# Kernel optimization log

Hardware: AMD Instinct MI355X
Metric: run time of the kernel (lower is better)

Reference implementation:

```python
import jax, jax.numpy as jnp
import numpy as np

N, D = 8192, 128
KERNEL_SCALE = 1.0     # constant baseline for kernel_scale
INV_TEMP = 1.0         # constant baseline: 1 / temperature
EMBED_DECAY = 0.0


def cauchy_kernel(x, y, scale):
    """Pairwise log-Cauchy kernel: -log(1 + ||x_i - y_j||^2 / scale). Shape [N, N]."""
    sq = (jnp.sum(x * x, axis=-1, keepdims=True)
          + jnp.sum(y * y, axis=-1)[None, :]
          - 2.0 * (x @ y.T))
    sq = jnp.maximum(sq, 0.0)  # guard tiny negatives from cancellation
    return -jnp.log1p(sq / scale)


def remove_diagonal(m):
    """[N, N] -> [N, N-1] dropping the diagonal (strided-view trick)."""
    n = m.shape[0]
    return m.reshape(-1)[1:].reshape(n - 1, n + 1)[:, :-1].reshape(n, n - 1)


def setup_inputs() -> dict:
    key = jax.random.key(0)
    k1, k2 = jax.random.split(key)
    z_x = jax.random.normal(k1, (N, D), dtype=jnp.float32)
    z_y = jax.random.normal(k2, (N, D), dtype=jnp.float32)
    return {"z_x": z_x, "z_y": z_y}


def reference(z_x, z_y):
    # pairwise log-likelihood-ratio logits
    logits = cauchy_kernel(z_x, z_y, KERNEL_SCALE) * INV_TEMP  # [N, N]
    pos_logits = jnp.diagonal(logits)[:, None]                 # [N, 1]
    neg_logits = remove_diagonal(logits)                       # [N, N-1]

    # "batch" baseline: log-mean-exp over all negative logits (scalar)
    log_baseline = jax.nn.logsumexp(neg_logits) - jnp.log(jnp.float32(neg_logits.size))

    pos_c = pos_logits - log_baseline
    neg_c = neg_logits - log_baseline

    # "kld" divergence (NCE/NWJ form): attraction on positives, exp-repulsion on negatives
    attraction = -jnp.mean(pos_c)
    repulsion = jnp.mean(jnp.exp(neg_c))

    # embedding prior = diagonal of kernel(z_y, zeros_like(z_y)) -> per-row log-density at origin
    embedding_prior = -jnp.log1p(jnp.sum(z_y * z_y, axis=-1) / KERNEL_SCALE)  # [N]
    embedding_decay = -EMBED_DECAY * jnp.mean(embedding_prior)

    loss = attraction + repulsion + embedding_decay
    return (jnp.mean(pos_logits), jnp.mean(neg_logits), log_baseline, loss)
```

## Files before the change

### kernel.cpp

```cpp
#include <hip/hip_runtime.h>
#include <hip/hip_bf16.h>

#define NN 8192
#define DD 128
#define NTB 64
#define STRIP 8

using floatx4 = __attribute__((ext_vector_type(4))) float;
using shortx8 = __attribute__((ext_vector_type(8))) short;
typedef unsigned short ushort_t;

typedef __attribute__((address_space(1))) const unsigned GlbU32;
typedef __attribute__((address_space(3))) unsigned LdsU32;

__device__ __forceinline__ unsigned bf16pair(float lo, float hi) {
    unsigned ulo = __float_as_uint(lo);
    ulo = (ulo + 0x7FFFu + ((ulo >> 16) & 1u)) >> 16;
    unsigned uhi = __float_as_uint(hi);
    uhi = (uhi + 0x7FFFu + ((uhi >> 16) & 1u)) & 0xFFFF0000u;
    return uhi | ulo;
}

__global__ void prep_kernel(const float* __restrict__ x, const float* __restrict__ y,
                            ushort_t* __restrict__ xb, ushort_t* __restrict__ yb,
                            float* __restrict__ xx, float* __restrict__ yy) {
    const int tid = threadIdx.x;
    const int r = blockIdx.x * 16 + (tid >> 4);
    const int c = tid & 15;
    const int sc = c ^ (r & 7);

    {
        const float4* xv = reinterpret_cast<const float4*>(x) + r * 32 + c * 2;
        const float4 a = xv[0], b = xv[1];
        uint4 u;
        u.x = bf16pair(a.x, a.y); u.y = bf16pair(a.z, a.w);
        u.z = bf16pair(b.x, b.y); u.w = bf16pair(b.z, b.w);
        reinterpret_cast<uint4*>(xb)[r * 16 + sc] = u;
        float s = a.x*a.x + a.y*a.y + a.z*a.z + a.w*a.w
                + b.x*b.x + b.y*b.y + b.z*b.z + b.w*b.w;
        #pragma unroll
        for (int off = 8; off; off >>= 1) s += __shfl_xor(s, off);
        if (c == 0) xx[r] = s;
    }
    {
        const float4* yv = reinterpret_cast<const float4*>(y) + r * 32 + c * 2;
        const float4 a = yv[0], b = yv[1];
        uint4 u;
        u.x = bf16pair(a.x, a.y); u.y = bf16pair(a.z, a.w);
        u.z = bf16pair(b.x, b.y); u.w = bf16pair(b.z, b.w);
        reinterpret_cast<uint4*>(yb)[r * 16 + sc] = u;
        float s = a.x*a.x + a.y*a.y + a.z*a.z + a.w*a.w
                + b.x*b.x + b.y*b.y + b.z*b.z + b.w*b.w;
        #pragma unroll
        for (int off = 8; off; off >>= 1) s += __shfl_xor(s, off);
        if (c == 0) yy[r] = s;
    }
}

__global__ __launch_bounds__(512, 4) void
tile_kernel(const ushort_t* __restrict__ xb, const ushort_t* __restrict__ yb,
            const float* __restrict__ xx, const float* __restrict__ yy,
            float* __restrict__ partials) {
    __shared__ __align__(16) ushort_t Bs[2][128 * DD];
    __shared__ float red[8][4];

    const int strip = blockIdx.x >> 6;
    const int by    = blockIdx.x & 63;
    const int bx0   = strip * STRIP;
    const int tid = threadIdx.x;
    const int wv = tid >> 6, lane = tid & 63;
    const int l15 = lane & 15, kq = lane >> 4;
    const int wr = (wv >> 1) * 32;
    const int wc = (wv & 1) * 64;
    const int lr = lane >> 4, lc = (lane & 15) * 8;

    #pragma unroll
    for (int it = 0; it < 4; ++it) {
        const int rbase = wv * 16 + it * 4;
        const ushort_t* gb = yb + ((size_t)(bx0 * 128 + rbase) + lr) * DD + lc;
        __builtin_amdgcn_global_load_lds((GlbU32*)gb, (LdsU32*)(&Bs[0][rbase * DD]), 16, 0, 0);
    }

    shortx8 a_reg[4][2];
    {
        const shortx8* xv = reinterpret_cast<const shortx8*>(xb);
        #pragma unroll
        for (int m = 0; m < 2; ++m) {
            const int ra = by * 128 + wr + m * 16 + l15;
            #pragma unroll
            for (int kk = 0; kk < 4; ++kk)
                a_reg[kk][m] = xv[ra * 16 + ((kk * 4 + kq) ^ (ra & 7))];
        }
    }
    float xv1[2][4];
    const int r0 = wr + kq * 4;
    #pragma unroll
    for (int m = 0; m < 2; ++m)
        #pragma unroll
        for (int j = 0; j < 4; ++j)
            xv1[m][j] = xx[by * 128 + r0 + m * 16 + j] + 1.0f;

    float s_l2 = 0.f, s_e = 0.f, p_l2 = 0.f, p_e = 0.f;

    __syncthreads();

    for (int t = 0; t < STRIP; ++t) {
        const int bx = bx0 + t;
        const int cur = t & 1;

        if (t + 1 < STRIP) {
            #pragma unroll
            for (int it = 0; it < 4; ++it) {
                const int rbase = wv * 16 + it * 4;
                const ushort_t* gb = yb + ((size_t)((bx + 1) * 128 + rbase) + lr) * DD + lc;
                __builtin_amdgcn_global_load_lds((GlbU32*)gb, (LdsU32*)(&Bs[cur ^ 1][rbase * DD]), 16, 0, 0);
            }
        }

        floatx4 acc[2][4];
        #pragma unroll
        for (int m = 0; m < 2; ++m)
            #pragma unroll
            for (int n = 0; n < 4; ++n)
                acc[m][n] = (floatx4){0.f, 0.f, 0.f, 0.f};

        const char* Bb = reinterpret_cast<const char*>(&Bs[cur][0]);
        #pragma unroll
        for (int kk = 0; kk < 4; ++kk) {
            shortx8 b[4];
            #pragma unroll
            for (int n = 0; n < 4; ++n) {
                const int rb = wc + n * 16 + l15;
                b[n] = *reinterpret_cast<const shortx8*>(Bb + ((rb * 256 + kk * 64 + kq * 16) ^ ((rb & 7) << 4)));
            }
            #pragma unroll
            for (int m = 0; m < 2; ++m)
                #pragma unroll
                for (int n = 0; n < 4; ++n)
                    acc[m][n] = __builtin_amdgcn_mfma_f32_16x16x32_bf16(a_reg[kk][m], b[n], acc[m][n], 0, 0, 0);
        }

        float yv[4];
        #pragma unroll
        for (int n = 0; n < 4; ++n) yv[n] = yy[bx * 128 + wc + n * 16 + l15];

        if (bx == by) {
            #pragma unroll
            for (int m = 0; m < 2; ++m)
                #pragma unroll
                for (int n = 0; n < 4; ++n)
                    #pragma unroll
                    for (int j = 0; j < 4; ++j) {
                        const float tt = fmaxf(fmaf(-2.0f, acc[m][n][j], xv1[m][j] + yv[n]), 1.0f);
                        const float l2 = __builtin_amdgcn_logf(tt);
                        const float e  = __builtin_amdgcn_rcpf(tt);
                        s_l2 += l2; s_e += e;
                        if (r0 + m * 16 + j == wc + n * 16 + l15) { p_l2 += l2; p_e += e; }
                    }
        } else {
            #pragma unroll
            for (int m = 0; m < 2; ++m)
                #pragma unroll
                for (int half = 0; half < 2; ++half) {
                    float prod = 1.0f;
                    #pragma unroll
                    for (int dn = 0; dn < 2; ++dn) {
                        const int n = half * 2 + dn;
                        #pragma unroll
                        for (int j = 0; j < 4; ++j) {
                            const float tt = fmaxf(fmaf(-2.0f, acc[m][n][j], xv1[m][j] + yv[n]), 1.0f);
                            prod *= tt;
                            s_e += __builtin_amdgcn_rcpf(tt);
                        }
                    }
                    s_l2 += __builtin_amdgcn_logf(prod);
                }
        }
        __syncthreads();
    }

    #pragma unroll
    for (int off = 32; off; off >>= 1) {
        s_l2 += __shfl_down(s_l2, off);
        s_e  += __shfl_down(s_e,  off);
        p_l2 += __shfl_down(p_l2, off);
        p_e  += __shfl_down(p_e,  off);
    }
    if (lane == 0) {
        red[wv][0] = s_l2; red[wv][1] = s_e; red[wv][2] = p_l2; red[wv][3] = p_e;
    }
    __syncthreads();
    if (tid < 4) {
        float v = 0.f;
        #pragma unroll
        for (int w = 0; w < 8; ++w) v += red[w][tid];
        partials[blockIdx.x * 4 + tid] = v;
    }
}

__global__ void finalize_kernel(const float* __restrict__ partials, int nblocks,
                                float* __restrict__ out) {
    float4 v = {0.f, 0.f, 0.f, 0.f};
    for (int i = threadIdx.x; i < nblocks; i += 256) {
        const float4 p = reinterpret_cast<const float4*>(partials)[i];
        v.x += p.x; v.y += p.y; v.z += p.z; v.w += p.w;
    }
    #pragma unroll
    for (int off = 32; off; off >>= 1) {
        v.x += __shfl_down(v.x, off);
        v.y += __shfl_down(v.y, off);
        v.z += __shfl_down(v.z, off);
        v.w += __shfl_down(v.w, off);
    }
    __shared__ float red[4][4];
    const int wv = threadIdx.x >> 6, lane = threadIdx.x & 63;
    if (lane == 0) { red[wv][0] = v.x; red[wv][1] = v.y; red[wv][2] = v.z; red[wv][3] = v.w; }
    __syncthreads();
    if (threadIdx.x == 0) {
        double Sl2 = 0, Se = 0, Pl2 = 0, Pe = 0;
        for (int w = 0; w < 4; ++w) {
            Sl2 += red[w][0]; Se += red[w][1]; Pl2 += red[w][2]; Pe += red[w][3];
        }
        const double LN2 = 0.6931471805599453;
        const double Sl = -LN2 * Sl2;
        const double Pl = -LN2 * Pl2;
        const double Nd = (double)NN;
        const double Md = Nd * (Nd - 1.0);
        const double mean_pos = Pl / Nd;
        const double mean_neg = (Sl - Pl) / Md;
        const double sumexp_neg = Se - Pe;
        const double lb = log(sumexp_neg) - log(Md);
        const double repulsion = sumexp_neg / (Md * exp(lb));
        const double loss = -(mean_pos - lb) + repulsion;
        out[0] = (float)mean_pos;
        out[1] = (float)mean_neg;
        out[2] = (float)lb;
        out[3] = (float)loss;
    }
}

extern "C" void kernel_launch(void* const* d_in, const int* in_sizes, int n_in,
                              void* d_out, int out_size, void* d_ws, size_t ws_size,
                              hipStream_t stream) {
    (void)in_sizes; (void)n_in; (void)out_size; (void)ws_size;
    const float* zx = (const float*)d_in[0];
    const float* zy = (const float*)d_in[1];
    float* out = (float*)d_out;
    char* ws = (char*)d_ws;

    float*    xx       = (float*)(ws);
    float*    yy       = (float*)(ws + (32 << 10));
    float*    partials = (float*)(ws + (64 << 10));
    ushort_t* xb       = (ushort_t*)(ws + (128 << 10));
    ushort_t* yb       = (ushort_t*)(ws + (128 << 10) + (2 << 20));

    const int nblocks = NTB * (NTB / STRIP);
    hipLaunchKernelGGL(prep_kernel, dim3(NN / 16), dim3(256), 0, stream, zx, zy, xb, yb, xx, yy);
    hipLaunchKernelGGL(tile_kernel, dim3(nblocks), dim3(512), 0, stream, xb, yb, xx, yy, partials);
    hipLaunchKernelGGL(finalize_kernel, dim3(1), dim3(256), 0, stream, partials, nblocks, out);
}
```

Before: 43.04 us.

## Reshape warp tile to 64x32 and vectorize epilogue accumulators

Changes the per-wave output tile from 32x64 to 64x32, so each wave keeps four A fragments in registers and reads only two B fragments from LDS per k-step. This halves LDS reads per wave. The epilogue now loads the x norms each tile as float4 from an SGPR-pinned pointer instead of holding them in registers across the loop, accumulates reciprocals in a vector, and splits the log sum into two accumulators to shorten dependency chains. The larger A register footprint raises register pressure under the 512x4 launch bounds.

```diff
diff --git a/kernel.cpp b/kernel.cpp
--- a/kernel.cpp
+++ b/kernel.cpp
@@ -70,8 +70,8 @@
     const int tid = threadIdx.x;
     const int wv = tid >> 6, lane = tid & 63;
     const int l15 = lane & 15, kq = lane >> 4;
-    const int wr = (wv >> 1) * 32;
-    const int wc = (wv & 1) * 64;
+    const int wr = (wv >> 2) * 64;
+    const int wc = (wv & 3) * 32;
     const int lr = lane >> 4, lc = (lane & 15) * 8;
 
     #pragma unroll
@@ -81,26 +81,21 @@
         __builtin_amdgcn_global_load_lds((GlbU32*)gb, (LdsU32*)(&Bs[0][rbase * DD]), 16, 0, 0);
     }
 
-    shortx8 a_reg[4][2];
+    shortx8 a_reg[4][4];
     {
-        const shortx8* xv = reinterpret_cast<const shortx8*>(xb);
-        #pragma unroll
-        for (int m = 0; m < 2; ++m) {
+        const shortx8* xv8 = reinterpret_cast<const shortx8*>(xb);
+        #pragma unroll
+        for (int m = 0; m < 4; ++m) {
             const int ra = by * 128 + wr + m * 16 + l15;
             #pragma unroll
             for (int kk = 0; kk < 4; ++kk)
-                a_reg[kk][m] = xv[ra * 16 + ((kk * 4 + kq) ^ (ra & 7))];
-        }
-    }
-    float xv1[2][4];
+                a_reg[kk][m] = xv8[ra * 16 + ((kk * 4 + kq) ^ (ra & 7))];
+        }
+    }
     const int r0 = wr + kq * 4;
-    #pragma unroll
-    for (int m = 0; m < 2; ++m)
-        #pragma unroll
-        for (int j = 0; j < 4; ++j)
-            xv1[m][j] = xx[by * 128 + r0 + m * 16 + j] + 1.0f;
-
-    float s_l2 = 0.f, s_e = 0.f, p_l2 = 0.f, p_e = 0.f;
+
+    floatx4 sev = {0.f, 0.f, 0.f, 0.f};
+    float sl2a = 0.f, sl2b = 0.f, p_l2 = 0.f, p_e = 0.f;
 
     __syncthreads();
 
@@ -117,68 +112,81 @@
             }
         }
 
-        floatx4 acc[2][4];
-        #pragma unroll
-        for (int m = 0; m < 2; ++m)
-            #pragma unroll
-            for (int n = 0; n < 4; ++n)
-                acc[m][n] = (floatx4){0.f, 0.f, 0.f, 0.f};
+        const float yv0 = yy[bx * 128 + wc + l15];
+        const float yv1 = yy[bx * 128 + wc + 16 + l15];
+
+        floatx4 acc[4][2];
+        #pragma unroll
+        for (int m = 0; m < 4; ++m) {
+            acc[m][0] = (floatx4){0.f, 0.f, 0.f, 0.f};
+            acc[m][1] = (floatx4){0.f, 0.f, 0.f, 0.f};
+        }
 
         const char* Bb = reinterpret_cast<const char*>(&Bs[cur][0]);
+        const int rb0 = wc + l15, rb1 = wc + 16 + l15;
+        const int sw0 = (rb0 & 7) << 4, sw1 = (rb1 & 7) << 4;
         #pragma unroll
         for (int kk = 0; kk < 4; ++kk) {
-            shortx8 b[4];
-            #pragma unroll
-            for (int n = 0; n < 4; ++n) {
-                const int rb = wc + n * 16 + l15;
-                b[n] = *reinterpret_cast<const shortx8*>(Bb + ((rb * 256 + kk * 64 + kq * 16) ^ ((rb & 7) << 4)));
+            const int off = kk * 64 + kq * 16;
+            const shortx8 b0 = *reinterpret_cast<const shortx8*>(Bb + rb0 * 256 + (off ^ sw0));
+            const shortx8 b1 = *reinterpret_cast<const shortx8*>(Bb + rb1 * 256 + (off ^ sw1));
+            #pragma unroll
+            for (int m = 0; m < 4; ++m) {
+                acc[m][0] = __builtin_amdgcn_mfma_f32_16x16x32_bf16(a_reg[kk][m], b0, acc[m][0], 0, 0, 0);
+                acc[m][1] = __builtin_amdgcn_mfma_f32_16x16x32_bf16(a_reg[kk][m], b1, acc[m][1], 0, 0, 0);
             }
-            #pragma unroll
-            for (int m = 0; m < 2; ++m)
+        }
+
+        const float* xp = xx + by * 128;
+        asm volatile("" : "+s"(xp));
+        floatx4 xvm[4];
+        #pragma unroll
+        for (int m = 0; m < 4; ++m)
+            xvm[m] = *reinterpret_cast<const floatx4*>(xp + wr + m * 16 + kq * 4);
+
+        const float y0p = yv0 + 1.0f, y1p = yv1 + 1.0f;
+
+        if (bx == by) {
+            #pragma unroll
+            for (int m = 0; m < 4; ++m)
                 #pragma unroll
-                for (int n = 0; n < 4; ++n)
-                    acc[m][n] = __builtin_amdgcn_mfma_f32_16x16x32_bf16(a_reg[kk][m], b[n], acc[m][n], 0, 0, 0);
-        }
-
-        float yv[4];
-        #pragma unroll
-        for (int n = 0; n < 4; ++n) yv[n] = yy[bx * 128 + wc + n * 16 + l15];
-
-        if (bx == by) {
-            #pragma unroll
-            for (int m = 0; m < 2; ++m)
-                #pragma unroll
-                for (int n = 0; n < 4; ++n)
+                for (int n = 0; n < 2; ++n)
                     #pragma unroll
                     for (int j = 0; j < 4; ++j) {
-                        const float tt = fmaxf(fmaf(-2.0f, acc[m][n][j], xv1[m][j] + yv[n]), 1.0f);
+                        const float pre = xvm[m][j] + (n ? y1p : y0p);
+                        const float tt = fmaxf(fmaf(-2.0f, acc[m][n][j], pre), 1.0f);
                         const float l2 = __builtin_amdgcn_logf(tt);
                         const float e  = __builtin_amdgcn_rcpf(tt);
-                        s_l2 += l2; s_e += e;
+                        sl2a += l2; sev[j] += e;
                         if (r0 + m * 16 + j == wc + n * 16 + l15) { p_l2 += l2; p_e += e; }
                     }
         } else {
             #pragma unroll
-            for (int m = 0; m < 2; ++m)
+            for (int m = 0; m < 4; ++m) {
+                floatx4 t0, t1, e0, e1;
                 #pragma unroll
-                for (int half = 0; half < 2; ++half) {
-                    float prod = 1.0f;
-                    #pragma unroll
-                    for (int dn = 0; dn < 2; ++dn) {
-                        const int n = half * 2 + dn;
-                        #pragma unroll
-                        for (int j = 0; j < 4; ++j) {
-                            const float tt = fmaxf(fmaf(-2.0f, acc[m][n][j], xv1[m][j] + yv[n]), 1.0f);
-                            prod *= tt;
-                            s_e += __builtin_amdgcn_rcpf(tt);
-                        }
-                    }
-                    s_l2 += __builtin_amdgcn_logf(prod);
+                for (int j = 0; j < 4; ++j) {
+                    t0[j] = fmaxf(fmaf(-2.0f, acc[m][0][j], xvm[m][j] + y0p), 1.0f);
+                    t1[j] = fmaxf(fmaf(-2.0f, acc[m][1][j], xvm[m][j] + y1p), 1.0f);
                 }
+                #pragma unroll
+                for (int j = 0; j < 4; ++j) {
+                    e0[j] = __builtin_amdgcn_rcpf(t0[j]);
+                    e1[j] = __builtin_amdgcn_rcpf(t1[j]);
+                }
+                sev += e0;
+                sev += e1;
+                const float pr = ((t0[0] * t0[1]) * (t0[2] * t0[3]))
+                               * ((t1[0] * t1[1]) * (t1[2] * t1[3]));
+                if (m & 1) sl2b += __builtin_amdgcn_logf(pr);
+                else       sl2a += __builtin_amdgcn_logf(pr);
+            }
         }
         __syncthreads();
     }
 
+    float s_l2 = sl2a + sl2b;
+    float s_e  = sev[0] + sev[1] + sev[2] + sev[3];
     #pragma unroll
     for (int off = 32; off; off >>= 1) {
         s_l2 += __shfl_down(s_l2, off);
```

Result: slower. 72.03 us (+67.4%).

## Shrink column tiles to 64 with 4-wave blocks and restructure epilogue

Applied to the files above, without the earlier changes.

Changes the tile kernel from 512-thread blocks over 128x128 tiles to 256-thread blocks over 128x64 tiles, with each wave covering 32 rows by all 64 columns. This doubles the number of blocks and halves the LDS footprint per block, which is meant to raise occupancy and spread work more evenly across CUs. The epilogue is rewritten to vectorise the reciprocal accumulation, split the log sums into two independent chains, and load yy before the MFMA loop. The cost is more blocks, so each x A-fragment load and the per-block reduction are repeated more often.

```diff
diff --git a/kernel.cpp b/kernel.cpp
--- a/kernel.cpp
+++ b/kernel.cpp
@@ -3,8 +3,10 @@
 
 #define NN 8192
 #define DD 128
-#define NTB 64
+#define BCOLS 64
 #define STRIP 8
+#define NCT (NN / BCOLS)
+#define NBLK (64 * (NCT / STRIP))
 
 using floatx4 = __attribute__((ext_vector_type(4))) float;
 using shortx8 = __attribute__((ext_vector_type(8))) short;
@@ -57,50 +59,52 @@
     }
 }
 
-__global__ __launch_bounds__(512, 4) void
+__global__ __launch_bounds__(256, 4) void
 tile_kernel(const ushort_t* __restrict__ xb, const ushort_t* __restrict__ yb,
             const float* __restrict__ xx, const float* __restrict__ yy,
             float* __restrict__ partials) {
-    __shared__ __align__(16) ushort_t Bs[2][128 * DD];
-    __shared__ float red[8][4];
-
+    __shared__ __align__(16) ushort_t Bs[2][BCOLS * DD];
+    __shared__ float red[4][4];
+
+    const int by    = blockIdx.x & 63;
     const int strip = blockIdx.x >> 6;
-    const int by    = blockIdx.x & 63;
     const int bx0   = strip * STRIP;
     const int tid = threadIdx.x;
     const int wv = tid >> 6, lane = tid & 63;
     const int l15 = lane & 15, kq = lane >> 4;
-    const int wr = (wv >> 1) * 32;
-    const int wc = (wv & 1) * 64;
+    const int wr = wv * 32;
     const int lr = lane >> 4, lc = (lane & 15) * 8;
 
     #pragma unroll
     for (int it = 0; it < 4; ++it) {
         const int rbase = wv * 16 + it * 4;
-        const ushort_t* gb = yb + ((size_t)(bx0 * 128 + rbase) + lr) * DD + lc;
+        const ushort_t* gb = yb + ((size_t)(bx0 * BCOLS + rbase) + lr) * DD + lc;
         __builtin_amdgcn_global_load_lds((GlbU32*)gb, (LdsU32*)(&Bs[0][rbase * DD]), 16, 0, 0);
     }
 
     shortx8 a_reg[4][2];
     {
-        const shortx8* xv = reinterpret_cast<const shortx8*>(xb);
+        const shortx8* xv8 = reinterpret_cast<const shortx8*>(xb);
         #pragma unroll
         for (int m = 0; m < 2; ++m) {
             const int ra = by * 128 + wr + m * 16 + l15;
             #pragma unroll
             for (int kk = 0; kk < 4; ++kk)
-                a_reg[kk][m] = xv[ra * 16 + ((kk * 4 + kq) ^ (ra & 7))];
-        }
-    }
+                a_reg[kk][m] = xv8[ra * 16 + ((kk * 4 + kq) ^ (ra & 7))];
+        }
+    }
+    const int r0 = wr + kq * 4;
+
     float xv1[2][4];
-    const int r0 = wr + kq * 4;
-    #pragma unroll
-    for (int m = 0; m < 2; ++m)
-        #pragma unroll
-        for (int j = 0; j < 4; ++j)
-            xv1[m][j] = xx[by * 128 + r0 + m * 16 + j] + 1.0f;
-
-    float s_l2 = 0.f, s_e = 0.f, p_l2 = 0.f, p_e = 0.f;
+    #pragma unroll
+    for (int m = 0; m < 2; ++m) {
+        const floatx4 v = *reinterpret_cast<const floatx4*>(xx + by * 128 + wr + m * 16 + kq * 4);
+        #pragma unroll
+        for (int j = 0; j < 4; ++j) xv1[m][j] = v[j] + 1.0f;
+    }
+
+    floatx4 sev = {0.f, 0.f, 0.f, 0.f};
+    float sl2a = 0.f, sl2b = 0.f, p_l2 = 0.f, p_e = 0.f;
 
     __syncthreads();
 
@@ -112,11 +116,15 @@
             #pragma unroll
             for (int it = 0; it < 4; ++it) {
                 const int rbase = wv * 16 + it * 4;
-                const ushort_t* gb = yb + ((size_t)((bx + 1) * 128 + rbase) + lr) * DD + lc;
+                const ushort_t* gb = yb + ((size_t)((bx + 1) * BCOLS + rbase) + lr) * DD + lc;
                 __builtin_amdgcn_global_load_lds((GlbU32*)gb, (LdsU32*)(&Bs[cur ^ 1][rbase * DD]), 16, 0, 0);
             }
         }
 
+        float yv[4];
+        #pragma unroll
+        for (int n = 0; n < 4; ++n) yv[n] = yy[bx * BCOLS + n * 16 + l15];
+
         floatx4 acc[2][4];
         #pragma unroll
         for (int m = 0; m < 2; ++m)
@@ -127,11 +135,12 @@
         const char* Bb = reinterpret_cast<const char*>(&Bs[cur][0]);
         #pragma unroll
         for (int kk = 0; kk < 4; ++kk) {
+            const int off = kk * 64 + kq * 16;
             shortx8 b[4];
             #pragma unroll
             for (int n = 0; n < 4; ++n) {
-                const int rb = wc + n * 16 + l15;
-                b[n] = *reinterpret_cast<const shortx8*>(Bb + ((rb * 256 + kk * 64 + kq * 16) ^ ((rb & 7) << 4)));
+                const int rb = n * 16 + l15;
+                b[n] = *reinterpret_cast<const shortx8*>(Bb + rb * 256 + (off ^ ((rb & 7) << 4)));
             }
             #pragma unroll
             for (int m = 0; m < 2; ++m)
@@ -140,45 +149,52 @@
                     acc[m][n] = __builtin_amdgcn_mfma_f32_16x16x32_bf16(a_reg[kk][m], b[n], acc[m][n], 0, 0, 0);
         }
 
-        float yv[4];
-        #pragma unroll
-        for (int n = 0; n < 4; ++n) yv[n] = yy[bx * 128 + wc + n * 16 + l15];
-
-        if (bx == by) {
+        if ((bx >> 1) == by) {
             #pragma unroll
             for (int m = 0; m < 2; ++m)
                 #pragma unroll
                 for (int n = 0; n < 4; ++n)
                     #pragma unroll
                     for (int j = 0; j < 4; ++j) {
-                        const float tt = fmaxf(fmaf(-2.0f, acc[m][n][j], xv1[m][j] + yv[n]), 1.0f);
+                        const float tt = fmaxf(fmaf(-2.0f, acc[m][n][j], xv1[m][j] + yv[n] + 1.0f - 1.0f), 1.0f);
                         const float l2 = __builtin_amdgcn_logf(tt);
                         const float e  = __builtin_amdgcn_rcpf(tt);
-                        s_l2 += l2; s_e += e;
-                        if (r0 + m * 16 + j == wc + n * 16 + l15) { p_l2 += l2; p_e += e; }
+                        sl2a += l2; sev[j] += e;
+                        if (by * 128 + r0 + m * 16 + j == bx * BCOLS + n * 16 + l15) { p_l2 += l2; p_e += e; }
                     }
         } else {
             #pragma unroll
-            for (int m = 0; m < 2; ++m)
-                #pragma unroll
-                for (int half = 0; half < 2; ++half) {
-                    float prod = 1.0f;
-                    #pragma unroll
-                    for (int dn = 0; dn < 2; ++dn) {
-                        const int n = half * 2 + dn;
-                        #pragma unroll
-                        for (int j = 0; j < 4; ++j) {
-                            const float tt = fmaxf(fmaf(-2.0f, acc[m][n][j], xv1[m][j] + yv[n]), 1.0f);
-                            prod *= tt;
-                            s_e += __builtin_amdgcn_rcpf(tt);
-                        }
-                    }
-                    s_l2 += __builtin_amdgcn_logf(prod);
+            for (int m = 0; m < 2; ++m) {
+                floatx4 t0, t1, e0, e1;
+                #pragma unroll
+                for (int j = 0; j < 4; ++j) {
+                    t0[j] = fmaxf(fmaf(-2.0f, acc[m][0][j], xv1[m][j] + yv[0]), 1.0f);
+                    t1[j] = fmaxf(fmaf(-2.0f, acc[m][1][j], xv1[m][j] + yv[1]), 1.0f);
                 }
+                #pragma unroll
+                for (int j = 0; j < 4; ++j) { e0[j] = __builtin_amdgcn_rcpf(t0[j]); e1[j] = __builtin_amdgcn_rcpf(t1[j]); }
+                sev += e0; sev += e1;
+                const float pr0 = ((t0[0] * t0[1]) * (t0[2] * t0[3]))
+                                * ((t1[0] * t1[1]) * (t1[2] * t1[3]));
+                #pragma unroll
+                for (int j = 0; j < 4; ++j) {
+                    t0[j] = fmaxf(fmaf(-2.0f, acc[m][2][j], xv1[m][j] + yv[2]), 1.0f);
+                    t1[j] = fmaxf(fmaf(-2.0f, acc[m][3][j], xv1[m][j] + yv[3]), 1.0f);
+                }
+                #pragma unroll
+                for (int j = 0; j < 4; ++j) { e0[j] = __builtin_amdgcn_rcpf(t0[j]); e1[j] = __builtin_amdgcn_rcpf(t1[j]); }
+                sev += e0; sev += e1;
+                const float pr1 = ((t0[0] * t0[1]) * (t0[2] * t0[3]))
+                                * ((t1[0] * t1[1]) * (t1[2] * t1[3]));
+                if (m) { sl2a += __builtin_amdgcn_logf(pr0); sl2b += __builtin_amdgcn_logf(pr1); }
+                else   { sl2a += __builtin_amdgcn_logf(pr0); sl2b += __builtin_amdgcn_logf(pr1); }
+            }
         }
         __syncthreads();
     }
 
+    float s_l2 = sl2a + sl2b;
+    float s_e  = sev[0] + sev[1] + sev[2] + sev[3];
     #pragma unroll
     for (int off = 32; off; off >>= 1) {
         s_l2 += __shfl_down(s_l2, off);
@@ -193,7 +209,7 @@
     if (tid < 4) {
         float v = 0.f;
         #pragma unroll
-        for (int w = 0; w < 8; ++w) v += red[w][tid];
+        for (int w = 0; w < 4; ++w) v += red[w][tid];
         partials[blockIdx.x * 4 + tid] = v;
     }
 }
@@ -254,8 +270,7 @@
     ushort_t* xb       = (ushort_t*)(ws + (128 << 10));
     ushort_t* yb       = (ushort_t*)(ws + (128 << 10) + (2 << 20));
 
-    const int nblocks = NTB * (NTB / STRIP);
     hipLaunchKernelGGL(prep_kernel, dim3(NN / 16), dim3(256), 0, stream, zx, zy, xb, yb, xx, yy);
-    hipLaunchKernelGGL(tile_kernel, dim3(nblocks), dim3(512), 0, stream, xb, yb, xx, yy, partials);
-    hipLaunchKernelGGL(finalize_kernel, dim3(1), dim3(256), 0, stream, partials, nblocks, out);
-}
+    hipLaunchKernelGGL(tile_kernel, dim3(NBLK), dim3(256), 0, stream, xb, yb, xx, yy, partials);
+    hipLaunchKernelGGL(finalize_kernel, dim3(1), dim3(256), 0, stream, partials, NBLK, out);
+}
```

Measured after the change: 66.84 us. 55.3% more time.
